# Kernel tuning notes

Measured on AMD Instinct MI355X. Metric: run time of the kernel, lower is better.

## Reference

```python
import jax, jax.numpy as jnp
import numpy as np

N = 10000
E = 160000
IN_DIM = 128
HID = 128
HEADS = 8
INT_DIM = 512
OUT_DIM = 3
NEG_SLOPE = 0.2


def gat_conv(x, src, dst, W, a_src, a_dst, b, heads, ch):
    # x: [N, F_in]; W: [F_in, heads*ch]; a_src/a_dst: [heads, ch]; b: [heads*ch]
    n = x.shape[0]
    h = (x @ W).reshape(n, heads, ch)                      # [N,H,C]
    alpha_src = jnp.einsum('nhc,hc->nh', h, a_src)         # [N,H]
    alpha_dst = jnp.einsum('nhc,hc->nh', h, a_dst)         # [N,H]
    e = jax.nn.leaky_relu(alpha_src[src] + alpha_dst[dst], NEG_SLOPE)  # [E,H]
    # segment softmax over incoming edges of each dst node
    emax = jax.ops.segment_max(e, dst, num_segments=n)     # [N,H]
    ee = jnp.exp(e - emax[dst])
    denom = jax.ops.segment_sum(ee, dst, num_segments=n)   # [N,H]
    alpha = ee / (denom[dst] + 1e-16)                      # [E,H]
    msg = h[src] * alpha[:, :, None]                       # [E,H,C]
    out = jax.ops.segment_sum(msg, dst, num_segments=n)    # [N,H,C]
    return out.reshape(n, heads * ch) + b


def setup_inputs() -> dict:
    key = jax.random.key(0)
    ks = jax.random.split(key, 20)

    def glorot(k, shape):
        fan = shape[0] + shape[-1]
        s = jnp.sqrt(6.0 / fan)
        return jax.random.uniform(k, shape, jnp.float32, -s, s)

    x = jax.random.normal(ks[0], (N, IN_DIM), jnp.float32)
    edge_index = jax.random.randint(ks[1], (2, E), 0, N, jnp.int32)
    return {
        'x': x,
        'edge_index': edge_index,
        'W1': glorot(ks[2], (IN_DIM, HEADS * HID)),
        'a_src1': glorot(ks[3], (HEADS, HID)),
        'a_dst1': glorot(ks[4], (HEADS, HID)),
        'b1': jnp.zeros((HEADS * HID,), jnp.float32),
        'W2': glorot(ks[5], (HEADS * HID, HEADS * HID)),
        'a_src2': glorot(ks[6], (HEADS, HID)),
        'a_dst2': glorot(ks[7], (HEADS, HID)),
        'b2': jnp.zeros((HEADS * HID,), jnp.float32),
        'W3': glorot(ks[8], (HEADS * HID, INT_DIM)),
        'a_src3': glorot(ks[9], (1, INT_DIM)),
        'a_dst3': glorot(ks[10], (1, INT_DIM)),
        'b3': jnp.zeros((INT_DIM,), jnp.float32),
        'Wl': glorot(ks[11], (INT_DIM, INT_DIM)),
        'bl': jnp.zeros((INT_DIM,), jnp.float32),
        'Wc': glorot(ks[12], (INT_DIM, OUT_DIM)),
        'bc': jnp.zeros((OUT_DIM,), jnp.float32),
    }


def reference(x, edge_index, W1, a_src1, a_dst1, b1, W2, a_src2, a_dst2, b2,
              W3, a_src3, a_dst3, b3, Wl, bl, Wc, bc):
    src, dst = edge_index[0], edge_index[1]
    # eval mode: dropout_edge and Dropout are identity
    h = gat_conv(x, src, dst, W1, a_src1, a_dst1, b1, HEADS, HID)
    h = jax.nn.relu(h)
    h = gat_conv(h, src, dst, W2, a_src2, a_dst2, b2, HEADS, HID)
    h = jax.nn.relu(h)
    h = gat_conv(h, src, dst, W3, a_src3, a_dst3, b3, 1, INT_DIM)
    h = jax.nn.relu(h)
    h = jax.nn.relu(h @ Wl + bl)
    return h @ Wc + bc
```

## Files before the change

### kernel.cpp

```cpp
#include <hip/hip_runtime.h>
#include <hip/hip_bf16.h>

#define NN 10000
#define EE 160000
#define IN_DIM 128
#define HID 128
#define HEADS 8
#define F1 (HEADS*HID)
#define INT_DIM 512
#define OUT_DIM 3
#define MPAD 10112

typedef __attribute__((ext_vector_type(4))) float f32x4;
typedef __attribute__((ext_vector_type(8))) _Float16 half8;
typedef __attribute__((ext_vector_type(4))) _Float16 half4;
typedef __attribute__((ext_vector_type(2))) _Float16 half2v;

#define WAVE_SYNC() do { asm volatile("s_waitcnt lgkmcnt(0)" ::: "memory"); \
                         __builtin_amdgcn_sched_barrier(0); } while(0)

__global__ __launch_bounds__(256) void count_kernel(const int* __restrict__ dst, int E, int* __restrict__ cnt){
    int e = blockIdx.x*256 + threadIdx.x;
    if(e < E) atomicAdd(&cnt[dst[e]], 1);
}

__global__ __launch_bounds__(256) void scan_kernel(const int* __restrict__ cnt, int* __restrict__ rowp,
                                                   int* __restrict__ cursor, int n){
    __shared__ int sh[256];
    __shared__ int stotal;
    int t = threadIdx.x;
    if(t==0) stotal = 0;
    __syncthreads();
    for(int base=0; base<n; base+=256){
        int i = base + t;
        int v = (i<n) ? cnt[i] : 0;
        sh[t] = v;
        __syncthreads();
        #pragma unroll
        for(int off=1; off<256; off<<=1){
            int add = (t>=off) ? sh[t-off] : 0;
            __syncthreads();
            sh[t] += add;
            __syncthreads();
        }
        int excl = sh[t] - v;
        if(i<n){ rowp[i] = stotal + excl; cursor[i] = stotal + excl; }
        int chunk_total = sh[255];
        __syncthreads();
        if(t==0) stotal += chunk_total;
        __syncthreads();
    }
    if(t==0) rowp[n] = stotal;
}

__global__ __launch_bounds__(256) void fill_kernel(const int* __restrict__ src, const int* __restrict__ dst,
                                                   int E, int* __restrict__ cursor, int* __restrict__ colsrc){
    int e = blockIdx.x*256 + threadIdx.x;
    if(e < E){
        int d = dst[e];
        int pos = atomicAdd(&cursor[d], 1);
        colsrc[pos] = src[e];
    }
}

__global__ __launch_bounds__(256) void splitT16_kernel(const float* __restrict__ B, _Float16* __restrict__ T,
                                                       int K, int N){
    __shared__ float tile[32][33];
    const int tx = threadIdx.x & 31, ty = threadIdx.x >> 5;
    const int n0 = blockIdx.x * 32, k0 = blockIdx.y * 32;
    #pragma unroll
    for(int i = 0; i < 32; i += 8)
        tile[ty + i][tx] = B[(size_t)(k0 + ty + i) * N + n0 + tx];
    __syncthreads();
    #pragma unroll
    for(int i = 0; i < 32; i += 8){
        int n = ty + i;
        T[(size_t)(n0 + n) * K + k0 + tx] = (_Float16)tile[tx][n];
    }
}

__global__ __launch_bounds__(256) void x16_kernel(const float* __restrict__ x, _Float16* __restrict__ x16, int n4){
    int i = blockIdx.x*256 + threadIdx.x;
    if(i >= n4) return;
    float4 v = ((const float4*)x)[i];
    half4 o = { (_Float16)v.x, (_Float16)v.y, (_Float16)v.z, (_Float16)v.w };
    ((half4*)x16)[i] = o;
}

__global__ __launch_bounds__(256) void aw1_kernel(const float* __restrict__ W1,
                                                  const float* __restrict__ a_src,
                                                  const float* __restrict__ a_dst,
                                                  float* __restrict__ aw){
    int idx = blockIdx.x*256 + threadIdx.x;
    if(idx >= 16*IN_DIM) return;
    int j = idx >> 7, k = idx & 127;
    int hj = j & 7;
    const float* av = (j < 8 ? a_src : a_dst) + hj*HID;
    const float* wr = W1 + (size_t)k*F1 + hj*HID;
    float s = 0.f;
    #pragma unroll 4
    for(int c = 0; c < HID; c++) s += av[c] * wr[c];
    aw[idx] = s;
}

__global__ __launch_bounds__(256) void alpha1_kernel(const float* __restrict__ x,
                                                     const float* __restrict__ aw,
                                                     float* __restrict__ asrc, float* __restrict__ adst){
    __shared__ float xs[16][128];
    __shared__ float aws[16][128];
    int t = threadIdx.x;
    int nb = blockIdx.x * 16;
    for(int i = t; i < 16*128; i += 256){
        xs[i >> 7][i & 127] = x[(size_t)nb*128 + i];
        aws[i >> 7][i & 127] = aw[i];
    }
    __syncthreads();
    int nl = t >> 4, j = t & 15;
    float s = 0.f;
    #pragma unroll 4
    for(int c = 0; c < 128; c++) s += xs[nl][c] * aws[j][c];
    int node = nb + nl;
    if(j < 8) asrc[node*8 + j] = s;
    else      adst[node*8 + (j-8)] = s;
}

__global__ __launch_bounds__(256) void agg1_kernel(const _Float16* __restrict__ x16,
                                                   const float* __restrict__ asrc,
                                                   const float* __restrict__ adst,
                                                   const int* __restrict__ rowp,
                                                   const int* __restrict__ colsrc,
                                                   _Float16* __restrict__ oa){
    const int w = threadIdx.x >> 6, l = threadIdx.x & 63;
    const int node = blockIdx.x*4 + w;
    __shared__ float sh_ee[4][64][8];
    int beg = rowp[node], end = rowp[node+1];
    float rd = adst[node*8 + (l & 7)];
    float acc0[8], acc1[8];
    #pragma unroll
    for(int h=0;h<8;h++){ acc0[h]=0.f; acc1[h]=0.f; }
    float dpart = 0.f;
    for(int base=beg; base<end; base+=64){
        int clen = min(64, end-base);
        WAVE_SYNC();
        int sreg = (l < clen) ? colsrc[base + l] : 0;
        for(int it=l; it<clen*8; it+=64){
            int j = it >> 3;
            int s = colsrc[base + j];
            float e = asrc[s*8 + (l & 7)] + rd;
            e = (e > 0.f) ? e : 0.2f*e;
            float ee = expf(e);
            sh_ee[w][j][l & 7] = ee;
            dpart += ee;
        }
        WAVE_SYNC();
        #pragma unroll 2
        for(int j=0;j<clen;j++){
            int s = __shfl(sreg, j);
            half2v xv = ((const half2v*)(x16 + (size_t)s*128))[l];
            float x0 = (float)xv[0], x1 = (float)xv[1];
            #pragma unroll
            for(int h=0;h<8;h++){
                float wt = sh_ee[w][j][h];
                acc0[h] += wt * x0;
                acc1[h] += wt * x1;
            }
        }
    }
    dpart += __shfl_xor(dpart, 8);
    dpart += __shfl_xor(dpart, 16);
    dpart += __shfl_xor(dpart, 32);
    #pragma unroll
    for(int h=0;h<8;h++){
        float dn = __shfl(dpart, h) + 1e-16f;
        half2v o = { (_Float16)(acc0[h]/dn), (_Float16)(acc1[h]/dn) };
        *(half2v*)(oa + (size_t)node*F1 + h*128 + 2*l) = o;
    }
}

__global__ __launch_bounds__(256) void agg2_kernel(const _Float16* __restrict__ hbuf,
                                                   const float* __restrict__ asrc,
                                                   const float* __restrict__ adst,
                                                   const int* __restrict__ rowp,
                                                   const int* __restrict__ colsrc,
                                                   const float* __restrict__ bias,
                                                   _Float16* __restrict__ oa){
    const int w = threadIdx.x >> 6, l = threadIdx.x & 63;
    const int h = blockIdx.x & 7;
    const int node = (blockIdx.x >> 3)*4 + w;
    int beg = rowp[node], end = rowp[node+1];
    float rd = adst[node*8 + h];
    float acc0 = 0.f, acc1 = 0.f;
    float dpart = 0.f;
    const _Float16* hb = hbuf + h*128 + 2*l;
    for(int base=beg; base<end; base+=64){
        int clen = min(64, end-base);
        int sreg = 0; float eereg = 0.f;
        if(l < clen){
            sreg = colsrc[base + l];
            float e = asrc[sreg*8 + h] + rd;
            e = (e > 0.f) ? e : 0.2f*e;
            eereg = expf(e);
            dpart += eereg;
        }
        int cpad = (clen + 7) & ~7;
        half2v v[8]; float wt[8];
        #pragma unroll
        for(int k=0;k<8;k++){
            int s = __shfl(sreg, k);
            wt[k] = __shfl(eereg, k);
            v[k] = *(const half2v*)(hb + (size_t)s*F1);
        }
        #pragma unroll 1
        for(int j0=0; j0<cpad; j0+=8){
            half2v nv[8]; float nw[8];
            const bool more = (j0+8 < cpad);
            if(more){
                #pragma unroll
                for(int k=0;k<8;k++){
                    int s = __shfl(sreg, j0+8+k);
                    nw[k] = __shfl(eereg, j0+8+k);
                    nv[k] = *(const half2v*)(hb + (size_t)s*F1);
                }
            }
            #pragma unroll
            for(int k=0;k<8;k++){
                acc0 += wt[k]*(float)v[k][0];
                acc1 += wt[k]*(float)v[k][1];
            }
            if(more){
                #pragma unroll
                for(int k=0;k<8;k++){ v[k]=nv[k]; wt[k]=nw[k]; }
            }
        }
    }
    #pragma unroll
    for(int off=1; off<64; off<<=1) dpart += __shfl_xor(dpart, off);
    float dn = dpart + 1e-16f;
    const int f = h*128 + 2*l;
    float2 bb = *(const float2*)(bias + f);
    half2v o = { (_Float16)fmaxf(acc0/dn + bb.x, 0.f),
                 (_Float16)fmaxf(acc1/dn + bb.y, 0.f) };
    *(half2v*)(oa + (size_t)node*F1 + f) = o;
}

__global__ __launch_bounds__(256) void agg3_kernel(const _Float16* __restrict__ hbuf,
                                                   const float* __restrict__ asrc,
                                                   const float* __restrict__ adst,
                                                   const int* __restrict__ rowp,
                                                   const int* __restrict__ colsrc,
                                                   const float* __restrict__ bias,
                                                   _Float16* __restrict__ oa){
    const int w = threadIdx.x >> 6, l = threadIdx.x & 63;
    const int i = blockIdx.x & 7;
    const int chunk = i & 3, sub = i >> 2;
    const int node = ((blockIdx.x >> 3)*2 + sub)*4 + w;
    int beg = rowp[node], end = rowp[node+1];
    float rd = adst[node];
    float acc0 = 0.f, acc1 = 0.f;
    float dpart = 0.f;
    const _Float16* hb = hbuf + chunk*128 + 2*l;
    for(int base=beg; base<end; base+=64){
        int clen = min(64, end-base);
        int sreg = 0; float eereg = 0.f;
        if(l < clen){
            sreg = colsrc[base + l];
            float e = asrc[sreg] + rd;
            e = (e > 0.f) ? e : 0.2f*e;
            eereg = expf(e);
            dpart += eereg;
        }
        int cpad = (clen + 7) & ~7;
        half2v v[8]; float wt[8];
        #pragma unroll
        for(int k=0;k<8;k++){
            int s = __shfl(sreg, k);
            wt[k] = __shfl(eereg, k);
            v[k] = *(const half2v*)(hb + (size_t)s*INT_DIM);
        }
        #pragma unroll 1
        for(int j0=0; j0<cpad; j0+=8){
            half2v nv[8]; float nw[8];
            const bool more = (j0+8 < cpad);
            if(more){
                #pragma unroll
                for(int k=0;k<8;k++){
                    int s = __shfl(sreg, j0+8+k);
                    nw[k] = __shfl(eereg, j0+8+k);
                    nv[k] = *(const half2v*)(hb + (size_t)s*INT_DIM);
                }
            }
            #pragma unroll
            for(int k=0;k<8;k++){
                acc0 += wt[k]*(float)v[k][0];
                acc1 += wt[k]*(float)v[k][1];
            }
            if(more){
                #pragma unroll
                for(int k=0;k<8;k++){ v[k]=nv[k]; wt[k]=nw[k]; }
            }
        }
    }
    #pragma unroll
    for(int off=1; off<64; off<<=1) dpart += __shfl_xor(dpart, off);
    float dn = dpart + 1e-16f;
    const int f = chunk*128 + 2*l;
    float2 bb = *(const float2*)(bias + f);
    half2v o = { (_Float16)fmaxf(acc0/dn + bb.x, 0.f),
                 (_Float16)fmaxf(acc1/dn + bb.y, 0.f) };
    *(half2v*)(oa + (size_t)node*INT_DIM + f) = o;
}

template<int FUSE>
__global__ __launch_bounds__(512, 4) void mfma16_gemm_kernel(
    const _Float16* __restrict__ A, int lda, int za,
    const _Float16* __restrict__ B, int ldb, int zb,
    const float* __restrict__ bias, _Float16* __restrict__ O,
    int ldc, int zc, int K, int gx)
{
    __shared__ _Float16 lA[2][128*32];
    __shared__ _Float16 lB[2][128*32];
    const int tid  = threadIdx.x;
    const int lane = tid & 63;
    const int w    = tid >> 6;
    const int wm   = w >> 2;
    const int wn   = w & 3;
    const int z    = blockIdx.z;

    const int nwg = gridDim.x;
    const int q = nwg >> 3, r = nwg & 7;
    const int xcd = blockIdx.x & 7, idx = blockIdx.x >> 3;
    const int wgid = (xcd < r ? xcd*(q+1) : r*(q+1) + (xcd-r)*q) + idx;
    const int row0 = (wgid / gx) * 128, col0 = (wgid % gx) * 128;

    f32x4 acc[4][2];
    #pragma unroll
    for(int i=0;i<4;i++)
        #pragma unroll
        for(int j=0;j<2;j++) acc[i][j] = (f32x4){0.f,0.f,0.f,0.f};

    const int rr1 = tid >> 2;
    const int ss1 = (tid & 3) ^ ((rr1 >> 1) & 3);
    const size_t aoff = (size_t)(row0 + rr1) * lda + (size_t)z*za + ss1 * 8;
    const size_t boff = (size_t)(col0 + rr1) * ldb + (size_t)z*zb + ss1 * 8;

    typedef __attribute__((address_space(3))) char lds_char;
    lds_char* dA = (lds_char*)(&lA[0][0]) + w*1024;
    lds_char* dB = (lds_char*)(&lB[0][0]) + w*1024;

    int arow[4], brow[2];
    const int slotx = ((lane >> 4) ^ ((lane >> 1) & 3)) << 4;
    #pragma unroll
    for(int i=0;i<4;i++)
        arow[i] = (wm*64 + i*16 + (lane & 15)) * 64 + slotx;
    #pragma unroll
    for(int j=0;j<2;j++)
        brow[j] = (wn*32 + j*16 + (lane & 15)) * 64 + slotx;

    #define GLDS(src, dst) __builtin_amdgcn_global_load_lds( \
        (__attribute__((address_space(1))) void*)(src), \
        (__attribute__((address_space(3))) void*)(dst), 16, 0, 0)
    GLDS(A + aoff, dA);
    GLDS(B + boff, dB);
    __syncthreads();

    #pragma unroll 1
    for(int k0 = 0, kb = 0; k0 < K; k0 += 32, kb ^= 1){
        if(k0 + 32 < K){
            const int nb = kb ^ 1;
            GLDS(A + aoff + k0 + 32, dA + nb*8192);
            GLDS(B + boff + k0 + 32, dB + nb*8192);
        }
        const char* pA = (const char*)(&lA[0][0]) + kb*8192;
        const char* pB = (const char*)(&lB[0][0]) + kb*8192;
        half8 af[4];
        #pragma unroll
        for(int i=0;i<4;i++) af[i] = *(const half8*)(pA + arow[i]);
        #pragma unroll
        for(int j=0;j<2;j++){
            half8 bf = *(const half8*)(pB + brow[j]);
            #pragma unroll
            for(int i=0;i<4;i++)
                acc[i][j] = __builtin_amdgcn_mfma_f32_16x16x32_f16(af[i], bf, acc[i][j], 0, 0, 0);
        }
        __syncthreads();
    }
    #undef GLDS

    #pragma unroll
    for(int i=0;i<4;i++){
        const int rr = row0 + wm*64 + i*16 + ((lane >> 4) << 2);
        #pragma unroll
        for(int j=0;j<2;j++){
            const int gc = z*zc + col0 + wn*32 + j*16 + (lane & 15);
            float b = FUSE ? bias[gc] : 0.f;
            #pragma unroll
            for(int rg=0;rg<4;rg++){
                float v = acc[i][j][rg];
                if(FUSE) v = fmaxf(v + b, 0.f);
                O[(size_t)(rr + rg) * ldc + gc] = (_Float16)v;
            }
        }
    }
}

__global__ __launch_bounds__(128) void alpha16_h8_kernel(const _Float16* __restrict__ hbuf,
                                                         const float* __restrict__ a_src,
                                                         const float* __restrict__ a_dst,
                                                         float* __restrict__ asrc, float* __restrict__ adst){
    int node = blockIdx.x;
    int t = threadIdx.x;
    half8 v = ((const half8*)(hbuf + (size_t)node*F1))[t];
    const float4* ap = (const float4*)(a_src + 8*t);
    const float4* dp = (const float4*)(a_dst + 8*t);
    float4 a0 = ap[0], a1 = ap[1];
    float4 d0 = dp[0], d1 = dp[1];
    float av[8] = {a0.x,a0.y,a0.z,a0.w, a1.x,a1.y,a1.z,a1.w};
    float dv[8] = {d0.x,d0.y,d0.z,d0.w, d1.x,d1.y,d1.z,d1.w};
    float ps = 0.f, pd = 0.f;
    #pragma unroll
    for(int k=0;k<8;k++){
        float f = (float)v[k];
        ps += f * av[k];
        pd += f * dv[k];
    }
    #pragma unroll
    for(int off=8; off; off>>=1){ ps += __shfl_down(ps, off); pd += __shfl_down(pd, off); }
    if((t & 15) == 0){
        asrc[(size_t)node*8 + (t>>4)] = ps;
        adst[(size_t)node*8 + (t>>4)] = pd;
    }
}

__global__ __launch_bounds__(128) void alpha16_h1_kernel(const _Float16* __restrict__ hbuf,
                                                         const float* __restrict__ a_src,
                                                         const float* __restrict__ a_dst,
                                                         float* __restrict__ asrc, float* __restrict__ adst){
    int node = blockIdx.x;
    int t = threadIdx.x;
    half4 v = ((const half4*)(hbuf + (size_t)node*INT_DIM))[t];
    float4 a = ((const float4*)a_src)[t];
    float4 d = ((const float4*)a_dst)[t];
    float ps = (float)v[0]*a.x + (float)v[1]*a.y + (float)v[2]*a.z + (float)v[3]*a.w;
    float pd = (float)v[0]*d.x + (float)v[1]*d.y + (float)v[2]*d.z + (float)v[3]*d.w;
    #pragma unroll
    for(int off=32; off; off>>=1){ ps += __shfl_down(ps, off); pd += __shfl_down(pd, off); }
    __shared__ float shs[2], shd[2];
    int wv = t >> 6;
    if((t & 63) == 0){ shs[wv] = ps; shd[wv] = pd; }
    __syncthreads();
    if(t == 0){
        asrc[node] = shs[0] + shs[1];
        adst[node] = shd[0] + shd[1];
    }
}

__global__ __launch_bounds__(256) void cls16_kernel(const _Float16* __restrict__ h, const float* __restrict__ Wc,
                                                    const float* __restrict__ bc, float* __restrict__ out, int n){
    int node = blockIdx.x*4 + (threadIdx.x >> 6);
    int lane = threadIdx.x & 63;
    if(node >= n) return;
    half8 v = ((const half8*)(h + (size_t)node*INT_DIM))[lane];
    float s0=0.f, s1=0.f, s2=0.f;
    #pragma unroll
    for(int k=0;k<8;k++){
        float f = (float)v[k];
        const float* wr = Wc + (8*lane + k)*3;
        s0 += f * wr[0];
        s1 += f * wr[1];
        s2 += f * wr[2];
    }
    #pragma unroll
    for(int off=32; off; off>>=1){
        s0 += __shfl_down(s0, off);
        s1 += __shfl_down(s1, off);
        s2 += __shfl_down(s2, off);
    }
    if(lane==0){
        out[(size_t)node*3+0] = s0 + bc[0];
        out[(size_t)node*3+1] = s1 + bc[1];
        out[(size_t)node*3+2] = s2 + bc[2];
    }
}

extern "C" void kernel_launch(void* const* d_in, const int* in_sizes, int n_in,
                              void* d_out, int out_size, void* d_ws, size_t ws_size,
                              hipStream_t stream){
    const float* x      = (const float*)d_in[0];
    const int*   ei     = (const int*)d_in[1];
    const float* W1     = (const float*)d_in[2];
    const float* a_src1 = (const float*)d_in[3];
    const float* a_dst1 = (const float*)d_in[4];
    const float* b1     = (const float*)d_in[5];
    const float* W2     = (const float*)d_in[6];
    const float* a_src2 = (const float*)d_in[7];
    const float* a_dst2 = (const float*)d_in[8];
    const float* b2     = (const float*)d_in[9];
    const float* W3     = (const float*)d_in[10];
    const float* a_src3 = (const float*)d_in[11];
    const float* a_dst3 = (const float*)d_in[12];
    const float* b3     = (const float*)d_in[13];
    const float* Wl     = (const float*)d_in[14];
    const float* bl     = (const float*)d_in[15];
    const float* Wc     = (const float*)d_in[16];
    const float* bc     = (const float*)d_in[17];
    float* out = (float*)d_out;

    const int* src = ei;
    const int* dst = ei + EE;

    char* p = (char*)d_ws;
    char* regA = p;  p += (size_t)MPAD*F1*4;
    char* regB = p;  p += (size_t)MPAD*F1*4;
    _Float16* wt16 = (_Float16*)p;  p += (size_t)F1*F1*2;
    _Float16* x16  = (_Float16*)p;  p += (size_t)NN*IN_DIM*2;
    float* aw1  = (float*)p;  p += 16*IN_DIM*4;
    float* asrc = (float*)p;  p += (size_t)NN*HEADS*4;
    float* adst = (float*)p;  p += (size_t)NN*HEADS*4;
    int* cnt    = (int*)p;    p += NN*4;
    int* rowp   = (int*)p;    p += (NN+1)*4;
    int* cursor = (int*)p;    p += NN*4;
    int* colsrc = (int*)p;    p += EE*4;

    _Float16* hA = (_Float16*)regA;
    _Float16* hB = (_Float16*)regB;

    hipMemsetAsync(cnt, 0, NN*sizeof(int), stream);
    count_kernel<<<(EE+255)/256, 256, 0, stream>>>(dst, EE, cnt);
    scan_kernel<<<1, 256, 0, stream>>>(cnt, rowp, cursor, NN);
    fill_kernel<<<(EE+255)/256, 256, 0, stream>>>(src, dst, EE, cursor, colsrc);

    x16_kernel<<<(NN*IN_DIM/4 + 255)/256, 256, 0, stream>>>(x, x16, NN*IN_DIM/4);
    splitT16_kernel<<<dim3(F1/32, IN_DIM/32), 256, 0, stream>>>(W1, wt16, IN_DIM, F1);
    aw1_kernel<<<8, 256, 0, stream>>>(W1, a_src1, a_dst1, aw1);
    alpha1_kernel<<<NN/16, 256, 0, stream>>>(x, aw1, asrc, adst);
    agg1_kernel<<<NN/4, 256, 0, stream>>>(x16, asrc, adst, rowp, colsrc, hA);
    mfma16_gemm_kernel<1><<<dim3(MPAD/128, 1, HEADS), 512, 0, stream>>>(
        hA, F1, 128,  wt16, IN_DIM, 128*IN_DIM,
        b1, hB, F1, 128,  IN_DIM, 1);

    splitT16_kernel<<<dim3(F1/32, F1/32), 256, 0, stream>>>(W2, wt16, F1, F1);
    mfma16_gemm_kernel<0><<<dim3((F1/128)*(MPAD/128), 1, 1), 512, 0, stream>>>(
        hB, F1, 0,  wt16, F1, 0,
        nullptr, hA, F1, 0,  F1, F1/128);
    alpha16_h8_kernel<<<NN, 128, 0, stream>>>(hA, a_src2, a_dst2, asrc, adst);
    agg2_kernel<<<(NN/4)*8, 256, 0, stream>>>(hA, asrc, adst, rowp, colsrc, b2, hB);

    splitT16_kernel<<<dim3(INT_DIM/32, F1/32), 256, 0, stream>>>(W3, wt16, F1, INT_DIM);
    mfma16_gemm_kernel<0><<<dim3((INT_DIM/128)*(MPAD/128), 1, 1), 512, 0, stream>>>(
        hB, F1, 0,  wt16, F1, 0,
        nullptr, hA, INT_DIM, 0,  F1, INT_DIM/128);
    alpha16_h1_kernel<<<NN, 128, 0, stream>>>(hA, a_src3, a_dst3, asrc, adst);
    agg3_kernel<<<(NN/8)*8, 256, 0, stream>>>(hA, asrc, adst, rowp, colsrc, b3, hB);

    splitT16_kernel<<<dim3(INT_DIM/32, INT_DIM/32), 256, 0, stream>>>(Wl, wt16, INT_DIM, INT_DIM);
    mfma16_gemm_kernel<1><<<dim3((INT_DIM/128)*(MPAD/128), 1, 1), 512, 0, stream>>>(
        hB, INT_DIM, 0,  wt16, INT_DIM, 0,
        bl, hA, INT_DIM, 0,  INT_DIM, INT_DIM/128);

    cls16_kernel<<<(NN+3)/4, 256, 0, stream>>>(hA, Wc, bc, out, NN);
}
```

Before: 299.4 us.

## Split wave into 4 edge groups with 16-byte vector gathers in agg2/agg3

The layer-2 and layer-3 aggregation kernels now have each wave split into four 16-lane groups. Each group handles a different edge and each lane loads 8 halves (16 bytes) instead of one half2 per lane per edge. The partial sums are then combined across groups with xor shuffles, and only group 0 writes the output. The aim is to issue fewer, wider gather loads and more edges in flight per instruction, at the cost of a shallower prefetch (one step instead of eight) and extra reduction shuffles.

```diff
diff --git a/kernel.cpp b/kernel.cpp
--- a/kernel.cpp
+++ b/kernel.cpp
@@ -187,11 +187,14 @@
     const int w = threadIdx.x >> 6, l = threadIdx.x & 63;
     const int h = blockIdx.x & 7;
     const int node = (blockIdx.x >> 3)*4 + w;
+    const int g = l >> 4, i = l & 15;
     int beg = rowp[node], end = rowp[node+1];
     float rd = adst[node*8 + h];
-    float acc0 = 0.f, acc1 = 0.f;
+    float acc[8];
+    #pragma unroll
+    for(int k=0;k<8;k++) acc[k]=0.f;
     float dpart = 0.f;
-    const _Float16* hb = hbuf + h*128 + 2*l;
+    const _Float16* hb = hbuf + h*128 + 8*i;
     for(int base=beg; base<end; base+=64){
         int clen = min(64, end-base);
         int sreg = 0; float eereg = 0.f;
@@ -202,45 +205,43 @@
             eereg = expf(e);
             dpart += eereg;
         }
-        int cpad = (clen + 7) & ~7;
-        half2v v[8]; float wt[8];
-        #pragma unroll
-        for(int k=0;k<8;k++){
-            int s = __shfl(sreg, k);
-            wt[k] = __shfl(eereg, k);
-            v[k] = *(const half2v*)(hb + (size_t)s*F1);
-        }
+        int cpad = (clen + 3) & ~3;
+        int s0 = __shfl(sreg, g);
+        float w0 = __shfl(eereg, g);
+        half8 v0 = *(const half8*)(hb + (size_t)s0*F1);
         #pragma unroll 1
-        for(int j0=0; j0<cpad; j0+=8){
-            half2v nv[8]; float nw[8];
-            const bool more = (j0+8 < cpad);
+        for(int j0=0; j0<cpad; j0+=4){
+            half8 nv; float nw = 0.f;
+            const bool more = (j0+4 < cpad);
             if(more){
-                #pragma unroll
-                for(int k=0;k<8;k++){
-                    int s = __shfl(sreg, j0+8+k);
-                    nw[k] = __shfl(eereg, j0+8+k);
-                    nv[k] = *(const half2v*)(hb + (size_t)s*F1);
-                }
+                int ns = __shfl(sreg, j0+4+g);
+                nw = __shfl(eereg, j0+4+g);
+                nv = *(const half8*)(hb + (size_t)ns*F1);
             }
             #pragma unroll
-            for(int k=0;k<8;k++){
-                acc0 += wt[k]*(float)v[k][0];
-                acc1 += wt[k]*(float)v[k][1];
-            }
-            if(more){
-                #pragma unroll
-                for(int k=0;k<8;k++){ v[k]=nv[k]; wt[k]=nw[k]; }
-            }
-        }
+            for(int k=0;k<8;k++) acc[k] += w0 * (float)v0[k];
+            if(more){ v0 = nv; w0 = nw; }
+        }
+    }
+    #pragma unroll
+    for(int k=0;k<8;k++){
+        acc[k] += __shfl_xor(acc[k], 16);
+        acc[k] += __shfl_xor(acc[k], 32);
     }
     #pragma unroll
     for(int off=1; off<64; off<<=1) dpart += __shfl_xor(dpart, off);
     float dn = dpart + 1e-16f;
-    const int f = h*128 + 2*l;
-    float2 bb = *(const float2*)(bias + f);
-    half2v o = { (_Float16)fmaxf(acc0/dn + bb.x, 0.f),
-                 (_Float16)fmaxf(acc1/dn + bb.y, 0.f) };
-    *(half2v*)(oa + (size_t)node*F1 + f) = o;
+    if(g == 0){
+        const int f = h*128 + 8*i;
+        float4 b0 = *(const float4*)(bias + f);
+        float4 b1 = *(const float4*)(bias + f + 4);
+        float bb[8] = {b0.x,b0.y,b0.z,b0.w, b1.x,b1.y,b1.z,b1.w};
+        half8 o;
+        #pragma unroll
+        for(int k=0;k<8;k++)
+            o[k] = (_Float16)fmaxf(acc[k]/dn + bb[k], 0.f);
+        *(half8*)(oa + (size_t)node*F1 + f) = o;
+    }
 }
 
 __global__ __launch_bounds__(256) void agg3_kernel(const _Float16* __restrict__ hbuf,
@@ -251,14 +252,17 @@
                                                    const float* __restrict__ bias,
                                                    _Float16* __restrict__ oa){
     const int w = threadIdx.x >> 6, l = threadIdx.x & 63;
-    const int i = blockIdx.x & 7;
-    const int chunk = i & 3, sub = i >> 2;
+    const int i7 = blockIdx.x & 7;
+    const int chunk = i7 & 3, sub = i7 >> 2;
     const int node = ((blockIdx.x >> 3)*2 + sub)*4 + w;
+    const int g = l >> 4, i = l & 15;
     int beg = rowp[node], end = rowp[node+1];
     float rd = adst[node];
-    float acc0 = 0.f, acc1 = 0.f;
+    float acc[8];
+    #pragma unroll
+    for(int k=0;k<8;k++) acc[k]=0.f;
     float dpart = 0.f;
-    const _Float16* hb = hbuf + chunk*128 + 2*l;
+    const _Float16* hb = hbuf + chunk*128 + 8*i;
     for(int base=beg; base<end; base+=64){
         int clen = min(64, end-base);
         int sreg = 0; float eereg = 0.f;
@@ -269,45 +273,43 @@
             eereg = expf(e);
             dpart += eereg;
         }
-        int cpad = (clen + 7) & ~7;
-        half2v v[8]; float wt[8];
-        #pragma unroll
-        for(int k=0;k<8;k++){
-            int s = __shfl(sreg, k);
-            wt[k] = __shfl(eereg, k);
-            v[k] = *(const half2v*)(hb + (size_t)s*INT_DIM);
-        }
+        int cpad = (clen + 3) & ~3;
+        int s0 = __shfl(sreg, g);
+        float w0 = __shfl(eereg, g);
+        half8 v0 = *(const half8*)(hb + (size_t)s0*INT_DIM);
         #pragma unroll 1
-        for(int j0=0; j0<cpad; j0+=8){
-            half2v nv[8]; float nw[8];
-            const bool more = (j0+8 < cpad);
+        for(int j0=0; j0<cpad; j0+=4){
+            half8 nv; float nw = 0.f;
+            const bool more = (j0+4 < cpad);
             if(more){
-                #pragma unroll
-                for(int k=0;k<8;k++){
-                    int s = __shfl(sreg, j0+8+k);
-                    nw[k] = __shfl(eereg, j0+8+k);
-                    nv[k] = *(const half2v*)(hb + (size_t)s*INT_DIM);
-                }
+                int ns = __shfl(sreg, j0+4+g);
+                nw = __shfl(eereg, j0+4+g);
+                nv = *(const half8*)(hb + (size_t)ns*INT_DIM);
             }
             #pragma unroll
-            for(int k=0;k<8;k++){
-                acc0 += wt[k]*(float)v[k][0];
-                acc1 += wt[k]*(float)v[k][1];
-            }
-            if(more){
-                #pragma unroll
-                for(int k=0;k<8;k++){ v[k]=nv[k]; wt[k]=nw[k]; }
-            }
-        }
+            for(int k=0;k<8;k++) acc[k] += w0 * (float)v0[k];
+            if(more){ v0 = nv; w0 = nw; }
+        }
+    }
+    #pragma unroll
+    for(int k=0;k<8;k++){
+        acc[k] += __shfl_xor(acc[k], 16);
+        acc[k] += __shfl_xor(acc[k], 32);
     }
     #pragma unroll
     for(int off=1; off<64; off<<=1) dpart += __shfl_xor(dpart, off);
     float dn = dpart + 1e-16f;
-    const int f = chunk*128 + 2*l;
-    float2 bb = *(const float2*)(bias + f);
-    half2v o = { (_Float16)fmaxf(acc0/dn + bb.x, 0.f),
-                 (_Float16)fmaxf(acc1/dn + bb.y, 0.f) };
-    *(half2v*)(oa + (size_t)node*INT_DIM + f) = o;
+    if(g == 0){
+        const int f = chunk*128 + 8*i;
+        float4 b0 = *(const float4*)(bias + f);
+        float4 b1 = *(const float4*)(bias + f + 4);
+        float bb[8] = {b0.x,b0.y,b0.z,b0.w, b1.x,b1.y,b1.z,b1.w};
+        half8 o;
+        #pragma unroll
+        for(int k=0;k<8;k++)
+            o[k] = (_Float16)fmaxf(acc[k]/dn + bb[k], 0.f);
+        *(half8*)(oa + (size_t)node*INT_DIM + f) = o;
+    }
 }
 
 template<int FUSE>
```

Result: no change. 301.1 us (+0.5%).
